# Kernel tuning notes

Measured on AMD Instinct MI355X. Metric: run time of the kernel, lower is better.

Reference implementation:

```python
import jax, jax.numpy as jnp
import numpy as np
import math

N, T, D_MODEL, H, D = 4, 2048, 1024, 16, 64


def setup_inputs() -> dict:
    key = jax.random.key(0)
    ks = jax.random.split(key, 12)
    s = 0.02
    return {
        "xq": jax.random.normal(ks[0], (N, T, D_MODEL), dtype=jnp.float32),
        "xk": jax.random.normal(ks[1], (N, T, D_MODEL), dtype=jnp.float32),
        "xv": jax.random.normal(ks[2], (N, T, D_MODEL), dtype=jnp.float32),
        "padding_mask": jnp.ones((N, T), dtype=jnp.int32),
        "Wq": jax.random.normal(ks[3], (D_MODEL, H * D), dtype=jnp.float32) * s,
        "bq": jnp.zeros((H * D,), dtype=jnp.float32),
        "Wk": jax.random.normal(ks[4], (D_MODEL, H * D), dtype=jnp.float32) * s,
        "bk": jnp.zeros((H * D,), dtype=jnp.float32),
        "Wv": jax.random.normal(ks[5], (D_MODEL, H * D), dtype=jnp.float32) * s,
        "bv": jnp.zeros((H * D,), dtype=jnp.float32),
        "Wo": jax.random.normal(ks[6], (H * D, D_MODEL), dtype=jnp.float32) * s,
        "bo": jnp.zeros((D_MODEL,), dtype=jnp.float32),
    }


def reference(xq, xk, xv, padding_mask, Wq, bq, Wk, bk, Wv, bv, Wo, bo):
    n, t_out, _ = xq.shape
    t_in = xk.shape[1]
    # projections
    Q = (xq @ Wq + bq).reshape(n, t_out, H, D).transpose(0, 2, 1, 3)  # [N,H,Tq,D]
    K = (xk @ Wk + bk).reshape(n, t_in, H, D).transpose(0, 2, 1, 3)   # [N,H,Tk,D]
    V = (xv @ Wv + bv).reshape(n, t_in, H, D).transpose(0, 2, 1, 3)
    scores = jnp.einsum("bhqd,bhkd->bhqk", Q, K) / math.sqrt(D)       # [N,H,Tq,Tk]
    neg_inf = jnp.float32(-jnp.inf)
    # padding mask: mask keys where padding_mask == 0
    scores = jnp.where(padding_mask[:, None, None, :] == 0, neg_inf, scores)
    # causal mask (tril of ones[max_len,max_len] sliced to [Tq,Tk])
    q_idx = jnp.arange(t_out)[:, None]
    k_idx = jnp.arange(t_in)[None, :]
    scores = jnp.where((k_idx <= q_idx)[None, None, :, :], scores, neg_inf)
    w = jax.nn.softmax(scores, axis=-1)
    attn = jnp.einsum("bhqk,bhkd->bhqd", w, V)                         # [N,H,Tq,D]
    attn = attn.transpose(0, 2, 1, 3).reshape(n, t_out, H * D)
    return attn @ Wo + bo
```

## Files before the change

### kernel.cpp

```cpp
#include <hip/hip_runtime.h>
#include <hip/hip_bf16.h>
#include <cstdint>

#define NB 4
#define TT 2048
#define DM 1024
#define NH 16
#define HD 64
#define QBLK 256
#define KVB 128

typedef __attribute__((ext_vector_type(8))) short bf16x8;
typedef __attribute__((ext_vector_type(4))) float f32x4;
typedef __attribute__((ext_vector_type(16))) float f32x16;
typedef __attribute__((ext_vector_type(4))) float float4v;
typedef __attribute__((ext_vector_type(4))) int i32x4;

static __device__ __forceinline__ unsigned short f2bf(float x) {
    unsigned int u = __float_as_uint(x);
    unsigned int r = (u + 0x7fffu + ((u >> 16) & 1u)) >> 16;
    return (unsigned short)r;
}
static __device__ __forceinline__ uint32_t pk2bf(float lo, float hi) {
    union { __hip_bfloat162 v; uint32_t u; } c;
    c.v = __float22bfloat162_rn(float2{lo, hi});
    return c.u;
}

#define GLOAD16(gp, lp) __builtin_amdgcn_global_load_lds(                 \
    (const __attribute__((address_space(1))) void*)(gp),                  \
    (__attribute__((address_space(3))) void*)(lp), 16, 0, 0)
#define BAR() asm volatile("s_barrier" ::: "memory")
#define WAITV8() asm volatile("s_waitcnt vmcnt(8)" ::: "memory")
#define WAITV4() asm volatile("s_waitcnt vmcnt(4)" ::: "memory")
#define WAITV0() asm volatile("s_waitcnt vmcnt(0)" ::: "memory")

__global__ __launch_bounds__(256) void k_prep(const float* __restrict__ W0,
                                              const float* __restrict__ W1,
                                              const float* __restrict__ W2,
                                              const float* __restrict__ W3,
                                              unsigned short* __restrict__ Wt,
                                              const float* __restrict__ sq,
                                              const float* __restrict__ sk,
                                              const float* __restrict__ sv,
                                              unsigned short* __restrict__ Xb,
                                              int n8) {
    const int z = blockIdx.z;
    const int tx = threadIdx.x, ty = threadIdx.y;
    if (z < 4) {
        __shared__ unsigned short tile[32][33];
        const float* W = (z == 0) ? W0 : (z == 1) ? W1 : (z == 2) ? W2 : W3;
        unsigned short* dst = Wt + (size_t)z * DM * DM;
        int kb = blockIdx.x * 32, nb = blockIdx.y * 32;
#pragma unroll
        for (int i = 0; i < 4; ++i)
            tile[ty + i * 8][tx] = f2bf(W[(size_t)(kb + ty + i * 8) * DM + nb + tx]);
        __syncthreads();
#pragma unroll
        for (int i = 0; i < 4; ++i)
            dst[(size_t)(nb + ty + i * 8) * DM + kb + tx] = tile[tx][ty + i * 8];
    } else {
        const int c = z - 4;
        const float* s = (c == 0) ? sq : (c == 1) ? sk : sv;
        unsigned short* d = Xb + (size_t)c * n8 * 8;
        const int tid = ty * 32 + tx;
        int i = (blockIdx.y * 32 + blockIdx.x) * 256 + tid;
        const int stride = 32 * 32 * 256;
        for (; i < n8; i += stride) {
            const float4v* sp = (const float4v*)(s + (size_t)i * 8);
            float4v v0 = sp[0], v1 = sp[1];
            uint4 o;
            o.x = pk2bf(v0[0], v0[1]);
            o.y = pk2bf(v0[2], v0[3]);
            o.z = pk2bf(v1[0], v1[1]);
            o.w = pk2bf(v1[2], v1[3]);
            *(uint4*)(d + (size_t)i * 8) = o;
        }
    }
}

template <int BATCHED>
__global__ __launch_bounds__(256) void k_gemm(const unsigned short* __restrict__ A0,
                                              const unsigned short* __restrict__ Bt0,
                                              const float* __restrict__ bias0,
                                              const float* __restrict__ bias1,
                                              const float* __restrict__ bias2,
                                              unsigned short* __restrict__ QKb,
                                              unsigned short* __restrict__ Vt,
                                              float* __restrict__ Cf,
                                              float scale0) {
    __shared__ __align__(16) char Asl[2][16384];
    __shared__ __align__(16) char Bsl[2][16384];
    const int tid = threadIdx.x;
    const int lane = tid & 63, wid = tid >> 6;
    const int lg = lane >> 4, lc = lane & 15;
    const int wm = wid >> 1, wn = wid & 1;
    const int m0 = blockIdx.x * 128, n0 = blockIdx.y * 128;
    const int z = BATCHED ? blockIdx.z : 0;

    const char* Ab = (const char*)(A0 + (size_t)z * NB * TT * DM);
    const char* Bb = (const char*)(Bt0 + (size_t)z * DM * DM);
    const float* bias = (z == 0) ? bias0 : (z == 1) ? bias1 : bias2;
    const float scale = (BATCHED && z != 0) ? 1.0f : scale0;

    f32x4 acc[4][4];
#pragma unroll
    for (int mi = 0; mi < 4; ++mi)
#pragma unroll
        for (int ni = 0; ni < 4; ++ni)
            acc[mi][ni] = (f32x4){0.f, 0.f, 0.f, 0.f};

    auto stage = [&](int buf, int k0) {
#pragma unroll
        for (int j = 0; j < 4; ++j) {
            const int row = j * 32 + (tid >> 3);
            const int swz = ((tid & 7) * 16) ^ ((row & 7) << 4);
            GLOAD16(Ab + (size_t)(m0 + row) * (DM * 2) + k0 * 2 + swz,
                    &Asl[buf][0] + j * 4096 + tid * 16);
            GLOAD16(Bb + (size_t)(n0 + row) * (DM * 2) + k0 * 2 + swz,
                    &Bsl[buf][0] + j * 4096 + tid * 16);
        }
    };

    stage(0, 0);
    __syncthreads();

    int cur = 0;
    for (int t = 0; t < DM / 64; ++t) {
        if (t + 1 < DM / 64) {
            stage(cur ^ 1, (t + 1) * 64);
            WAITV8();
        } else {
            WAITV0();
        }
        BAR();

#pragma unroll
        for (int kk = 0; kk < 2; ++kk) {
            bf16x8 af[4], bfr[4];
#pragma unroll
            for (int ni = 0; ni < 4; ++ni) {
                const int n = wn * 64 + ni * 16 + lc;
                bfr[ni] = *(const bf16x8*)(&Bsl[cur][0] + n * 128 +
                                           ((kk * 64 + lg * 16) ^ ((n & 7) << 4)));
            }
#pragma unroll
            for (int mi = 0; mi < 4; ++mi) {
                const int m = wm * 64 + mi * 16 + lc;
                af[mi] = *(const bf16x8*)(&Asl[cur][0] + m * 128 +
                                          ((kk * 64 + lg * 16) ^ ((m & 7) << 4)));
            }
            __builtin_amdgcn_s_setprio(1);
#pragma unroll
            for (int mi = 0; mi < 4; ++mi)
#pragma unroll
                for (int ni = 0; ni < 4; ++ni)
                    acc[mi][ni] = __builtin_amdgcn_mfma_f32_16x16x32_bf16(af[mi], bfr[ni],
                                                                          acc[mi][ni], 0, 0, 0);
            __builtin_amdgcn_s_setprio(0);
        }
        BAR();
        cur ^= 1;
    }

#pragma unroll
    for (int mi = 0; mi < 4; ++mi)
#pragma unroll
        for (int ni = 0; ni < 4; ++ni) {
            const int m = m0 + wm * 64 + mi * 16 + lg * 4;
            const int n = n0 + wn * 64 + ni * 16 + lc;
            float v[4];
#pragma unroll
            for (int r = 0; r < 4; ++r) v[r] = (acc[mi][ni][r] + bias[n]) * scale;
            if (!BATCHED) {
#pragma unroll
                for (int r = 0; r < 4; ++r) Cf[(size_t)(m + r) * DM + n] = v[r];
            } else {
                const int b = m >> 11, tl = m & (TT - 1), h = n >> 6, d = n & 63;
                if (z == 2) {
                    uint2 w;
                    w.x = pk2bf(v[0], v[1]);
                    w.y = pk2bf(v[2], v[3]);
                    *(uint2*)(Vt + ((size_t)(b * NH + h) * HD + d) * TT + tl) = w;
                } else {
#pragma unroll
                    for (int r = 0; r < 4; ++r)
                        QKb[(size_t)z * NB * NH * TT * HD +
                            (((size_t)b * NH + h) * TT + tl + r) * HD + d] = f2bf(v[r]);
                }
            }
        }
}

__global__ __launch_bounds__(512) void k_attn(const unsigned short* __restrict__ Qg,
                                              const unsigned short* __restrict__ Kg,
                                              const unsigned short* __restrict__ Vtg,
                                              const int* __restrict__ pm,
                                              unsigned short* __restrict__ Og) {
    __shared__ __align__(16) unsigned short Kl[2][KVB * HD];
    __shared__ __align__(16) unsigned short Vl[2][KVB * HD];
    __shared__ uint64_t pmbits[TT / 64];

    const int idx = blockIdx.x;
    const int half = idx >> 8, r5 = idx & 255;
    const int a = r5 & 3;
    const int qb = half ? (7 - a) : a;
    const int bh = r5 >> 2;
    const int b = bh >> 4, h = bh & 15;
    const int qbase = qb * QBLK;
    const int tid = threadIdx.x;
    const int wid = tid >> 6, lane = tid & 63;
    const int hi = lane >> 5, l31 = lane & 31;
    const int q0 = qbase + wid * 32;
    const int q = q0 + l31;

    const unsigned short* Qh = Qg + (size_t)bh * TT * HD;
    const char* Khb = (const char*)(Kg + (size_t)bh * TT * HD);
    const char* Vthb = (const char*)(Vtg + (size_t)bh * HD * TT);
    const int* pmb = pm + b * TT;

    char* const kdst = (char*)&Kl[0][0];
    char* const vdst = (char*)&Vl[0][0];

#define ASTAGE(buf, kv0_)                                                        \
    {                                                                            \
        _Pragma("unroll")                                                        \
        for (int p = 0; p < 2; ++p) {                                            \
            GLOAD16(Khb + (size_t)((kv0_) + p * 64 + lane) * 128 + wid * 16,     \
                    kdst + (buf) * 16384 + wid * 2048 + p * 1024 + lane * 16);   \
            GLOAD16(Vthb + (size_t)lane * 4096 + (size_t)(kv0_) * 2 + (p * 8 + wid) * 16, \
                    vdst + (buf) * 16384 + p * 8192 + wid * 1024 + lane * 16);   \
        }                                                                        \
    }

    ASTAGE(0, 0);

#pragma unroll
    for (int it = 0; it < 4; ++it) {
        const int g = wid + it * 8;
        unsigned long long msk = __ballot(pmb[g * 64 + lane] != 0);
        if (lane == 0) pmbits[g] = msk;
    }

    bf16x8 qf[4];
#pragma unroll
    for (int dd = 0; dd < 4; ++dd)
        qf[dd] = *(const bf16x8*)((const char*)Qh + (size_t)q * 128 + dd * 32 + hi * 16);

    f32x16 o0, o1;
#pragma unroll
    for (int r = 0; r < 16; ++r) { o0[r] = 0.f; o1[r] = 0.f; }
    float mrow = -INFINITY, msafe = -1.0e30f, lrow = 0.f;

    __syncthreads();

    const int nt = (qbase + QBLK) >> 7;
    int cur = 0;
    for (int t = 0; t < nt; ++t) {
        const int kv0 = t << 7;
        if (t + 1 < nt) {
            ASTAGE(cur ^ 1, kv0 + KVB);
            WAITV4();
        } else {
            WAITV0();
        }
        BAR();

        const char* kb = (const char*)&Kl[0][0] + cur * 16384;
        const char* vbp = (const char*)&Vl[0][0] + cur * 16384;

#pragma unroll
        for (int hh = 0; hh < 2; ++hh) {
            const int k0 = kv0 + hh * 64;
            if (k0 > q0 + 31) continue;

            const uint64_t vb = pmbits[k0 >> 6];
            const uint32_t pm0 = ((uint32_t)vb) >> (4 * hi);
            const uint32_t pm1 = ((uint32_t)(vb >> 32)) >> (4 * hi);
            const bool allvalid = (vb == ~0ull);
            const bool do2 = (k0 + 32 <= q0 + 31);
            const bool needmask = (k0 + 63 > q0) || !allvalid;
            const char* kbh = kb + hh * 1024;
            const char* vbh = vbp + hh * 8192;

            f32x16 st0, st1;
#pragma unroll
            for (int r = 0; r < 16; ++r) { st0[r] = 0.f; st1[r] = 0.f; }
            __builtin_amdgcn_s_setprio(1);
#pragma unroll
            for (int dd = 0; dd < 4; ++dd) {
                const char* kchunk = kbh + (dd * 2 + hi) * 2048;
                bf16x8 kf = *(const bf16x8*)(kchunk + l31 * 16);
                st0 = __builtin_amdgcn_mfma_f32_32x32x16_bf16(kf, qf[dd], st0, 0, 0, 0);
            }
            if (do2) {
#pragma unroll
                for (int dd = 0; dd < 4; ++dd) {
                    const char* kchunk = kbh + (dd * 2 + hi) * 2048;
                    bf16x8 kf = *(const bf16x8*)(kchunk + 512 + l31 * 16);
                    st1 = __builtin_amdgcn_mfma_f32_32x32x16_bf16(kf, qf[dd], st1, 0, 0, 0);
                }
            }
            __builtin_amdgcn_s_setprio(0);

            const int qr = q - k0 - 4 * hi;
            if (needmask) {
#pragma unroll
                for (int r = 0; r < 16; ++r) {
                    const int c = (r & 3) + 8 * (r >> 2);
                    st0[r] = (((pm0 >> c) & 1) && (c <= qr)) ? st0[r] : -INFINITY;
                }
                if (do2) {
#pragma unroll
                    for (int r = 0; r < 16; ++r) {
                        const int c = (r & 3) + 8 * (r >> 2);
                        st1[r] = (((pm1 >> c) & 1) && (c + 32 <= qr)) ? st1[r] : -INFINITY;
                    }
                }
            }

            float mloc = -INFINITY;
#pragma unroll
            for (int r = 0; r < 16; ++r) mloc = fmaxf(mloc, st0[r]);
            if (do2) {
#pragma unroll
                for (int r = 0; r < 16; ++r) mloc = fmaxf(mloc, st1[r]);
            }
            const float cmax = fmaxf(mloc, __shfl_xor(mloc, 32, 64));
            if (!__all(cmax - mrow <= 8.0f)) {
                const float mnew = fmaxf(mrow, cmax);
                const float ms = fmaxf(mnew, -1.0e30f);
                const float esc = __builtin_amdgcn_exp2f(mrow - ms);
#pragma unroll
                for (int r = 0; r < 16; ++r) { o0[r] *= esc; o1[r] *= esc; }
                lrow *= esc;
                mrow = mnew;
                msafe = ms;
            }

            float tot = 0.f;
#pragma unroll
            for (int r = 0; r < 16; ++r) {
                st0[r] = __builtin_amdgcn_exp2f(st0[r] - msafe);
                tot += st0[r];
            }
            if (do2) {
#pragma unroll
                for (int r = 0; r < 16; ++r) {
                    st1[r] = __builtin_amdgcn_exp2f(st1[r] - msafe);
                    tot += st1[r];
                }
            }
            lrow += tot + __shfl_xor(tot, 32, 64);

            __builtin_amdgcn_s_setprio(1);
#pragma unroll
            for (int kc = 0; kc < 2; ++kc) {
                uint32_t A0 = pk2bf(st0[kc * 8 + 0], st0[kc * 8 + 1]);
                uint32_t A1 = pk2bf(st0[kc * 8 + 2], st0[kc * 8 + 3]);
                uint32_t C0 = pk2bf(st0[kc * 8 + 4], st0[kc * 8 + 5]);
                uint32_t C1 = pk2bf(st0[kc * 8 + 6], st0[kc * 8 + 7]);
                uint32_t oA0 = __shfl_xor(A0, 32, 64), oA1 = __shfl_xor(A1, 32, 64);
                uint32_t oC0 = __shfl_xor(C0, 32, 64), oC1 = __shfl_xor(C1, 32, 64);
                i32x4 pf = {(int)(hi ? oC0 : A0), (int)(hi ? oC1 : A1),
                            (int)(hi ? C0 : oA0), (int)(hi ? C1 : oA1)};
                bf16x8 pb = *(bf16x8*)&pf;
                const char* vchunk = vbh + (kc * 2 + hi) * 1024;
                {
                    bf16x8 vf = *(const bf16x8*)(vchunk + l31 * 16);
                    o0 = __builtin_amdgcn_mfma_f32_32x32x16_bf16(vf, pb, o0, 0, 0, 0);
                }
                {
                    bf16x8 vf = *(const bf16x8*)(vchunk + 512 + l31 * 16);
                    o1 = __builtin_amdgcn_mfma_f32_32x32x16_bf16(vf, pb, o1, 0, 0, 0);
                }
            }
            if (do2) {
#pragma unroll
                for (int kc = 0; kc < 2; ++kc) {
                    uint32_t A0 = pk2bf(st1[kc * 8 + 0], st1[kc * 8 + 1]);
                    uint32_t A1 = pk2bf(st1[kc * 8 + 2], st1[kc * 8 + 3]);
                    uint32_t C0 = pk2bf(st1[kc * 8 + 4], st1[kc * 8 + 5]);
                    uint32_t C1 = pk2bf(st1[kc * 8 + 6], st1[kc * 8 + 7]);
                    uint32_t oA0 = __shfl_xor(A0, 32, 64), oA1 = __shfl_xor(A1, 32, 64);
                    uint32_t oC0 = __shfl_xor(C0, 32, 64), oC1 = __shfl_xor(C1, 32, 64);
                    i32x4 pf = {(int)(hi ? oC0 : A0), (int)(hi ? oC1 : A1),
                                (int)(hi ? C0 : oA0), (int)(hi ? C1 : oA1)};
                    bf16x8 pb = *(bf16x8*)&pf;
                    const char* vchunk = vbh + (4 + kc * 2 + hi) * 1024;
                    {
                        bf16x8 vf = *(const bf16x8*)(vchunk + l31 * 16);
                        o0 = __builtin_amdgcn_mfma_f32_32x32x16_bf16(vf, pb, o0, 0, 0, 0);
                    }
                    {
                        bf16x8 vf = *(const bf16x8*)(vchunk + 512 + l31 * 16);
                        o1 = __builtin_amdgcn_mfma_f32_32x32x16_bf16(vf, pb, o1, 0, 0, 0);
                    }
                }
            }
            __builtin_amdgcn_s_setprio(0);
        }
        BAR();
        cur ^= 1;
    }

    const float inv = (lrow > 0.f) ? (1.0f / lrow) : 0.f;
    unsigned short* orow = Og + ((size_t)(b * TT + q)) * DM + h * HD;
#pragma unroll
    for (int g4 = 0; g4 < 4; ++g4) {
        uint32_t w0 = pk2bf(o0[g4 * 4 + 0] * inv, o0[g4 * 4 + 1] * inv);
        uint32_t w1 = pk2bf(o0[g4 * 4 + 2] * inv, o0[g4 * 4 + 3] * inv);
        *(uint2*)(orow + g4 * 8 + 4 * hi) = make_uint2(w0, w1);
    }
#pragma unroll
    for (int g4 = 0; g4 < 4; ++g4) {
        uint32_t w0 = pk2bf(o1[g4 * 4 + 0] * inv, o1[g4 * 4 + 1] * inv);
        uint32_t w1 = pk2bf(o1[g4 * 4 + 2] * inv, o1[g4 * 4 + 3] * inv);
        *(uint2*)(orow + 32 + g4 * 8 + 4 * hi) = make_uint2(w0, w1);
    }
}

extern "C" void kernel_launch(void* const* d_in, const int* in_sizes, int n_in,
                              void* d_out, int out_size, void* d_ws, size_t ws_size,
                              hipStream_t stream) {
    const float* xq = (const float*)d_in[0];
    const float* xk = (const float*)d_in[1];
    const float* xv = (const float*)d_in[2];
    const int* pmask = (const int*)d_in[3];
    const float* Wq = (const float*)d_in[4];
    const float* bq = (const float*)d_in[5];
    const float* Wk = (const float*)d_in[6];
    const float* bk = (const float*)d_in[7];
    const float* Wv = (const float*)d_in[8];
    const float* bv = (const float*)d_in[9];
    const float* Wo = (const float*)d_in[10];
    const float* bo = (const float*)d_in[11];

    char* ws = (char*)d_ws;
    const size_t WT = (size_t)DM * DM * 2;
    const size_t QKV = (size_t)NB * NH * TT * HD * 2;
    unsigned short* WqT = (unsigned short*)(ws + 0 * WT);
    unsigned short* WoT = WqT + 3 * (size_t)DM * DM;
    unsigned short* Qb = (unsigned short*)(ws + 4 * WT);
    unsigned short* Kb = (unsigned short*)(ws + 4 * WT + QKV);
    unsigned short* Vt = (unsigned short*)(ws + 4 * WT + 2 * QKV);
    unsigned short* Ob = (unsigned short*)(ws + 4 * WT + 3 * QKV);
    unsigned short* Xb = (unsigned short*)(ws + 4 * WT + 4 * QKV);

    const float qscale = 0.125f * 1.44269504088896340736f;
    const int n8 = NB * TT * DM / 8;

    k_prep<<<dim3(32, 32, 7), dim3(32, 8), 0, stream>>>(Wq, Wk, Wv, Wo, WqT,
                                                        xq, xk, xv, Xb, n8);
    k_gemm<1><<<dim3(64, 8, 3), 256, 0, stream>>>(Xb, WqT, bq, bk, bv,
                                                  Qb, Vt, nullptr, qscale);

    k_attn<<<dim3((TT / QBLK) * NB * NH), 512, 0, stream>>>(Qb, Kb, Vt, pmask, Ob);

    k_gemm<0><<<dim3(64, 8, 1), 256, 0, stream>>>(Ob, WoT, bo, bo, bo,
                                                  nullptr, nullptr, (float*)d_out, 1.0f);
}
```

Baseline: 196.9 us.

## Use 256x256 tiles with 512 threads for the QKV projection GEMM

Replaces the batched QKV projection GEMM with a dedicated kernel using 256x256 output tiles, 8 waves per block and 64 KB LDS stages, to raise operand reuse per global load. It also specializes the output projection into its own kernel without the batched branches. The larger tiles cut the grid to 384 blocks and need 128 KB of LDS per block, which risks poor wave balance across the CUs and lower occupancy. The inner loop also adds extra barriers.

```diff
diff --git a/kernel.cpp b/kernel.cpp
--- a/kernel.cpp
+++ b/kernel.cpp
@@ -33,6 +33,7 @@
 #define BAR() asm volatile("s_barrier" ::: "memory")
 #define WAITV8() asm volatile("s_waitcnt vmcnt(8)" ::: "memory")
 #define WAITV4() asm volatile("s_waitcnt vmcnt(4)" ::: "memory")
+#define WAITV2() asm volatile("s_waitcnt vmcnt(2)" ::: "memory")
 #define WAITV0() asm volatile("s_waitcnt vmcnt(0)" ::: "memory")
 
 __global__ __launch_bounds__(256) void k_prep(const float* __restrict__ W0,
@@ -79,16 +80,130 @@
     }
 }
 
-template <int BATCHED>
-__global__ __launch_bounds__(256) void k_gemm(const unsigned short* __restrict__ A0,
-                                              const unsigned short* __restrict__ Bt0,
-                                              const float* __restrict__ bias0,
-                                              const float* __restrict__ bias1,
-                                              const float* __restrict__ bias2,
-                                              unsigned short* __restrict__ QKb,
-                                              unsigned short* __restrict__ Vt,
-                                              float* __restrict__ Cf,
-                                              float scale0) {
+__global__ __launch_bounds__(512) void k_gemm8(const unsigned short* __restrict__ A0,
+                                               const unsigned short* __restrict__ Bt0,
+                                               const float* __restrict__ bq,
+                                               const float* __restrict__ bk,
+                                               const float* __restrict__ bv,
+                                               unsigned short* __restrict__ QKb,
+                                               unsigned short* __restrict__ Vt,
+                                               float qscale) {
+    __shared__ __align__(16) char Asl[2][32768];
+    __shared__ __align__(16) char Bsl[2][32768];
+    const int tid = threadIdx.x;
+    const int lane = tid & 63, wid = tid >> 6;
+    const int lg = lane >> 4, lc = lane & 15;
+    const int wr = wid >> 2, wc = wid & 3;
+    const int m0 = blockIdx.x * 256, n0 = blockIdx.y * 256;
+    const int z = blockIdx.z;
+
+    const char* Ab = (const char*)(A0 + (size_t)z * NB * TT * DM);
+    const char* Bb = (const char*)(Bt0 + (size_t)z * DM * DM);
+    const float* bias = (z == 0) ? bq : (z == 1) ? bk : bv;
+    const float scale = (z == 0) ? qscale : 1.0f;
+
+    f32x4 acc[8][4];
+#pragma unroll
+    for (int mi = 0; mi < 8; ++mi)
+#pragma unroll
+        for (int ni = 0; ni < 4; ++ni)
+            acc[mi][ni] = (f32x4){0.f, 0.f, 0.f, 0.f};
+
+    const int srow = tid >> 3;
+    const int scol = (tid & 7) * 16;
+    auto stage = [&](int buf, int k0) {
+#pragma unroll
+        for (int j = 0; j < 4; ++j) {
+            const int row = j * 64 + srow;
+            const int swz = scol ^ ((row & 7) << 4);
+            GLOAD16(Ab + (size_t)(m0 + row) * (DM * 2) + k0 * 2 + swz,
+                    &Asl[buf][0] + j * 8192 + tid * 16);
+        }
+#pragma unroll
+        for (int j = 0; j < 4; ++j) {
+            const int row = j * 64 + srow;
+            const int swz = scol ^ ((row & 7) << 4);
+            GLOAD16(Bb + (size_t)(n0 + row) * (DM * 2) + k0 * 2 + swz,
+                    &Bsl[buf][0] + j * 8192 + tid * 16);
+        }
+    };
+
+    stage(0, 0);
+
+    int cur = 0;
+    for (int t = 0; t < DM / 64; ++t) {
+        if (t + 1 < DM / 64) {
+            stage(cur ^ 1, (t + 1) * 64);
+            WAITV8();
+        } else {
+            WAITV0();
+        }
+        BAR();
+
+        bf16x8 bfr[4][2];
+#pragma unroll
+        for (int ni = 0; ni < 4; ++ni)
+#pragma unroll
+            for (int kk = 0; kk < 2; ++kk) {
+                const int n = wc * 64 + ni * 16 + lc;
+                bfr[ni][kk] = *(const bf16x8*)(&Bsl[cur][0] + n * 128 +
+                                               ((kk * 64 + lg * 16) ^ ((n & 7) << 4)));
+            }
+
+#pragma unroll
+        for (int p = 0; p < 4; ++p) {
+            bf16x8 af[2][2];
+#pragma unroll
+            for (int mi2 = 0; mi2 < 2; ++mi2)
+#pragma unroll
+                for (int kk = 0; kk < 2; ++kk) {
+                    const int m = wr * 128 + (p * 2 + mi2) * 16 + lc;
+                    af[mi2][kk] = *(const bf16x8*)(&Asl[cur][0] + m * 128 +
+                                                   ((kk * 64 + lg * 16) ^ ((m & 7) << 4)));
+                }
+            __builtin_amdgcn_s_setprio(1);
+#pragma unroll
+            for (int mi2 = 0; mi2 < 2; ++mi2)
+#pragma unroll
+                for (int ni = 0; ni < 4; ++ni)
+#pragma unroll
+                    for (int kk = 0; kk < 2; ++kk)
+                        acc[p * 2 + mi2][ni] = __builtin_amdgcn_mfma_f32_16x16x32_bf16(
+                            af[mi2][kk], bfr[ni][kk], acc[p * 2 + mi2][ni], 0, 0, 0);
+            __builtin_amdgcn_s_setprio(0);
+            BAR();
+        }
+        cur ^= 1;
+    }
+
+#pragma unroll
+    for (int mi = 0; mi < 8; ++mi)
+#pragma unroll
+        for (int ni = 0; ni < 4; ++ni) {
+            const int m = m0 + wr * 128 + mi * 16 + lg * 4;
+            const int n = n0 + wc * 64 + ni * 16 + lc;
+            float v[4];
+#pragma unroll
+            for (int r = 0; r < 4; ++r) v[r] = (acc[mi][ni][r] + bias[n]) * scale;
+            const int b = m >> 11, tl = m & (TT - 1), h = n >> 6, d = n & 63;
+            if (z == 2) {
+                uint2 w;
+                w.x = pk2bf(v[0], v[1]);
+                w.y = pk2bf(v[2], v[3]);
+                *(uint2*)(Vt + ((size_t)(b * NH + h) * HD + d) * TT + tl) = w;
+            } else {
+#pragma unroll
+                for (int r = 0; r < 4; ++r)
+                    QKb[(size_t)z * NB * NH * TT * HD +
+                        (((size_t)b * NH + h) * TT + tl + r) * HD + d] = f2bf(v[r]);
+            }
+        }
+}
+
+__global__ __launch_bounds__(256) void k_gemm_o(const unsigned short* __restrict__ A,
+                                                const unsigned short* __restrict__ Bt,
+                                                const float* __restrict__ bias,
+                                                float* __restrict__ C) {
     __shared__ __align__(16) char Asl[2][16384];
     __shared__ __align__(16) char Bsl[2][16384];
     const int tid = threadIdx.x;
@@ -96,12 +211,9 @@
     const int lg = lane >> 4, lc = lane & 15;
     const int wm = wid >> 1, wn = wid & 1;
     const int m0 = blockIdx.x * 128, n0 = blockIdx.y * 128;
-    const int z = BATCHED ? blockIdx.z : 0;
-
-    const char* Ab = (const char*)(A0 + (size_t)z * NB * TT * DM);
-    const char* Bb = (const char*)(Bt0 + (size_t)z * DM * DM);
-    const float* bias = (z == 0) ? bias0 : (z == 1) ? bias1 : bias2;
-    const float scale = (BATCHED && z != 0) ? 1.0f : scale0;
+
+    const char* Ab = (const char*)A;
+    const char* Bb = (const char*)Bt;
 
     f32x4 acc[4][4];
 #pragma unroll
@@ -166,30 +278,13 @@
 #pragma unroll
     for (int mi = 0; mi < 4; ++mi)
 #pragma unroll
-        for (int ni = 0; ni < 4; ++ni) {
-            const int m = m0 + wm * 64 + mi * 16 + lg * 4;
-            const int n = n0 + wn * 64 + ni * 16 + lc;
-            float v[4];
-#pragma unroll
-            for (int r = 0; r < 4; ++r) v[r] = (acc[mi][ni][r] + bias[n]) * scale;
-            if (!BATCHED) {
-#pragma unroll
-                for (int r = 0; r < 4; ++r) Cf[(size_t)(m + r) * DM + n] = v[r];
-            } else {
-                const int b = m >> 11, tl = m & (TT - 1), h = n >> 6, d = n & 63;
-                if (z == 2) {
-                    uint2 w;
-                    w.x = pk2bf(v[0], v[1]);
-                    w.y = pk2bf(v[2], v[3]);
-                    *(uint2*)(Vt + ((size_t)(b * NH + h) * HD + d) * TT + tl) = w;
-                } else {
-#pragma unroll
-                    for (int r = 0; r < 4; ++r)
-                        QKb[(size_t)z * NB * NH * TT * HD +
-                            (((size_t)b * NH + h) * TT + tl + r) * HD + d] = f2bf(v[r]);
-                }
-            }
-        }
+        for (int ni = 0; ni < 4; ++ni)
+#pragma unroll
+            for (int r = 0; r < 4; ++r) {
+                int m = m0 + wm * 64 + mi * 16 + lg * 4 + r;
+                int n = n0 + wn * 64 + ni * 16 + lc;
+                C[(size_t)m * DM + n] = acc[mi][ni][r] + bias[n];
+            }
 }
 
 __global__ __launch_bounds__(512) void k_attn(const unsigned short* __restrict__ Qg,
@@ -452,11 +547,9 @@
 
     k_prep<<<dim3(32, 32, 7), dim3(32, 8), 0, stream>>>(Wq, Wk, Wv, Wo, WqT,
                                                         xq, xk, xv, Xb, n8);
-    k_gemm<1><<<dim3(64, 8, 3), 256, 0, stream>>>(Xb, WqT, bq, bk, bv,
-                                                  Qb, Vt, nullptr, qscale);
+    k_gemm8<<<dim3(32, 4, 3), 512, 0, stream>>>(Xb, WqT, bq, bk, bv, Qb, Vt, qscale);
 
     k_attn<<<dim3((TT / QBLK) * NB * NH), 512, 0, stream>>>(Qb, Kb, Vt, pmask, Ob);
 
-    k_gemm<0><<<dim3(64, 8, 1), 256, 0, stream>>>(Ob, WoT, bo, bo, bo,
-                                                  nullptr, nullptr, (float*)d_out, 1.0f);
-}
+    k_gemm_o<<<dim3(64, 8), 256, 0, stream>>>(Ob, WoT, bo, (float*)d_out);
+}
```

Measured after the change: 208.3 us. 1.06x slower.
